# Kernel tuning notes

Measured on AMD Instinct MI355X. Metric: run time of the kernel, lower is better.

Reference implementation:

```python
import jax, jax.numpy as jnp
import numpy as np

E = 1024      # hidden_size
H = 16        # num_heads
D = E // H    # head_dim = 64
WIN = 256     # window_size
STRIDE = 128
G = 1         # global_tokens
B = 2
L = 4097      # seq_len; local_seq_len = 4096 tiles exactly into 31 windows


def setup_inputs() -> dict:
    key = jax.random.key(0)
    ks = jax.random.split(key, 9)
    s = 0.02
    return {
        "hidden_states": jax.random.normal(ks[0], (B, L, E), jnp.float32),
        "Wq": jax.random.normal(ks[1], (E, E), jnp.float32) * s,
        "bq": jnp.zeros((E,), jnp.float32),
        "Wk": jax.random.normal(ks[2], (E, E), jnp.float32) * s,
        "bk": jnp.zeros((E,), jnp.float32),
        "Wv": jax.random.normal(ks[3], (E, E), jnp.float32) * s,
        "bv": jnp.zeros((E,), jnp.float32),
        "Wo": jax.random.normal(ks[4], (E, E), jnp.float32) * s,
        "bo": jnp.zeros((E,), jnp.float32),
    }


def reference(hidden_states, Wq, bq, Wk, bk, Wv, bv, Wo, bo):
    b, seq_len, e = hidden_states.shape
    scale = 1.0 / jnp.sqrt(jnp.asarray(D, hidden_states.dtype))

    q = (hidden_states @ Wq + bq).reshape(b, seq_len, H, D)
    k = (hidden_states @ Wk + bk).reshape(b, seq_len, H, D)
    v = (hidden_states @ Wv + bv).reshape(b, seq_len, H, D)

    # ---- global tokens attend to the full sequence ----
    qg = q[:, :G]                                        # [b, G, H, D]
    gw = jnp.einsum('bghd,bshd->bhgs', qg, k) * scale    # [b, H, G, L]
    gp = jax.nn.softmax(gw, axis=-1)
    gctx = jnp.einsum('bhgs,bshd->bghd', gp, v).reshape(b, G, e)

    # ---- local windowed attention (overlapping strided windows) ----
    ql, kl, vl = q[:, G:], k[:, G:], v[:, G:]
    Lc = seq_len - G                                     # 4096
    num_windows = max(1, (Lc - WIN) // STRIDE + 1)       # 31
    starts = jnp.arange(num_windows) * STRIDE
    widx = starts[:, None] + jnp.arange(WIN)             # [W, w] window indices

    qw = ql[:, widx]                                     # [b, W, w, H, D]
    kw = kl[:, widx]
    vw = vl[:, widx]
    aw = jnp.einsum('bwqhd,bwkhd->bwhqk', qw, kw) * scale  # [b, W, H, w, w]
    ap = jax.nn.softmax(aw, axis=-1)
    ctx = jnp.einsum('bwhqk,bwkhd->bwqhd', ap, vw)       # [b, W, w, H, D]
    ctx = ctx.reshape(b, num_windows * WIN, e)

    flat = widx.reshape(-1)                              # [W*w]
    local = jnp.zeros((b, Lc, e), hidden_states.dtype).at[:, flat].add(ctx)
    counts = jnp.zeros((Lc,), hidden_states.dtype).at[flat].add(1.0)
    counts = jnp.maximum(counts, 1.0)
    local = local / counts[None, :, None]                # average over overlaps

    out = jnp.concatenate([gctx, local], axis=1)         # [b, L, E]
    return out @ Wo + bo
```

## Files before the change

kernel.cpp:

```cpp
#include <hip/hip_runtime.h>

typedef unsigned short u16;
typedef unsigned int u32;
typedef __bf16 bf16x8 __attribute__((ext_vector_type(8)));
typedef float f4_t __attribute__((ext_vector_type(4)));

#define E_DIM 1024
#define L_TOT 4097
#define B_SZ 2
#define M_ROWS 8194
#define NWIN 31
#define HHEADS 16
#define GCHUNKS 17

__device__ __forceinline__ float b2f(u16 v) {
  union { u32 u; float f; } x; x.u = ((u32)v) << 16; return x.f;
}
__device__ __forceinline__ u16 f2b(float f) {
  union { float f; u32 u; } x; x.f = f;
  u32 r = (x.u + 0x7FFFu + ((x.u >> 16) & 1u)) >> 16;
  return (u16)r;
}
__device__ __forceinline__ f4_t mfma16(bf16x8 a, bf16x8 b, f4_t c) {
  return __builtin_amdgcn_mfma_f32_16x16x32_bf16(a, b, c, 0, 0, 0);
}
__device__ __forceinline__ u32 cvtpk(float lo, float hi) {
  u32 r;
  asm volatile("v_cvt_pk_bf16_f32 %0, %1, %2" : "=v"(r) : "v"(lo), "v"(hi));
  return r;
}

#define GLOAD16(gp, lp)                                                              \
  __builtin_amdgcn_global_load_lds(                                                  \
      (const __attribute__((address_space(1))) u32*)(gp),                            \
      (__attribute__((address_space(3))) u32*)(lp), 16, 0, 0)

#define WAITVM(N) asm volatile("s_waitcnt vmcnt(" #N ")" ::: "memory")
#define WAITLGKM asm volatile("s_waitcnt lgkmcnt(0)" ::: "memory")
#define SCHEDB __builtin_amdgcn_sched_barrier(0)

__global__ __launch_bounds__(256) void prep_kernel(const float* __restrict__ hs,
                                                   u16* __restrict__ hsb,
                                                   const float* __restrict__ w0,
                                                   const float* __restrict__ w1,
                                                   const float* __restrict__ w2,
                                                   const float* __restrict__ w3,
                                                   u16* __restrict__ wtb) {
  int bid = blockIdx.x;
  if (bid < M_ROWS) {
    int i = bid * 256 + threadIdx.x;
    float4 v = ((const float4*)hs)[i];
    u16 o[4] = {f2b(v.x), f2b(v.y), f2b(v.z), f2b(v.w)};
    *(uint2*)(hsb + (size_t)i * 4) = *(uint2*)o;
  } else {
    int idx2 = bid - M_ROWS;
    int bz = idx2 >> 10;
    int rem = idx2 & 1023;
    int bx = rem & 31, by = rem >> 5;
    const float* src = bz == 0 ? w0 : bz == 1 ? w1 : bz == 2 ? w2 : w3;
    u16* dst = wtb + (size_t)bz * E_DIM * E_DIM;
    __shared__ float tile[32][33];
    int tx = threadIdx.x & 31, ty = threadIdx.x >> 5;
    int x = bx * 32 + tx;
    int y0 = by * 32;
    for (int j = ty; j < 32; j += 8) tile[j][tx] = src[(size_t)(y0 + j) * E_DIM + x];
    __syncthreads();
    for (int j = ty; j < 32; j += 8)
      dst[(size_t)(bx * 32 + j) * E_DIM + by * 32 + tx] = f2b(tile[tx][j]);
  }
}

template <int MODE>
__device__ __forceinline__ void gemmC_body(const u16* __restrict__ A,
                                           const u16* __restrict__ Wt,
                                           const float* __restrict__ b0,
                                           const float* __restrict__ b1,
                                           const float* __restrict__ b2,
                                           void* __restrict__ outBase,
                                           int M) {
  __shared__ __align__(16) char smraw[34816];
  u16* sA = (u16*)smraw;
  u16* sB = sA + 2 * 4096;
  u16* epi16 = (u16*)smraw;
  float* epi32 = (float*)smraw;

  int orig = blockIdx.x;
  int xcd = orig & 7, l = orig >> 3;
  int mt, nt;
  if (MODE == 0) {
    if (l < 192) { mt = (xcd << 3) + (l & 7); nt = l >> 3; }
    else         { mt = 64; nt = xcd * 3 + (l - 192); }
  } else {
    if (l < 64)  { mt = (xcd << 3) + (l & 7); nt = l >> 3; }
    else         { mt = 64; nt = xcd; }
  }
  int m0 = mt * 128, n0 = nt * 128;

  int t = threadIdx.x, lane = t & 63, w = t >> 6;
  int wr = w >> 1, wc = w & 1;
  int lr = lane & 15, g = lane >> 4;

  int ssrc = (((t & 3) ^ ((t >> 3) & 3)) << 3);
  const u16* pa[2];
  const u16* pb[2];
#pragma unroll
  for (int c = 0; c < 2; c++) {
    int ra = m0 + c * 64 + (t >> 2);
    if (ra >= M) ra = M - 1;
    pa[c] = A + (size_t)ra * 1024 + ssrc;
    pb[c] = Wt + (size_t)(n0 + c * 64 + (t >> 2)) * 1024 + ssrc;
  }
  int wb = w * 512;

#define STAGE(bf, ks)                                              \
  {                                                                \
    GLOAD16(pa[0] + (ks) * 32, sA + (bf) * 4096 + wb);             \
    GLOAD16(pa[1] + (ks) * 32, sA + (bf) * 4096 + 2048 + wb);      \
    GLOAD16(pb[0] + (ks) * 32, sB + (bf) * 4096 + wb);             \
    GLOAD16(pb[1] + (ks) * 32, sB + (bf) * 4096 + 2048 + wb);      \
  }

  int swz = ((g ^ ((lr >> 1) & 3)) << 3);
  int arow0 = wr * 64 + lr;
  int brow0 = wc * 64 + lr;

  f4_t acc[4][4] = {};

  STAGE(0, 0);
  STAGE(1, 1);
  WAITVM(4);
  __builtin_amdgcn_s_barrier();
  SCHEDB;

#pragma unroll 2
  for (int ks = 0; ks < 32; ++ks) {
    int bf = ks & 1;
    int base = bf * 4096;
    bf16x8 av[4], bv[4];
#pragma unroll
    for (int i = 0; i < 4; i++)
      av[i] = *(const bf16x8*)&sA[base + (arow0 + i * 16) * 32 + swz];
#pragma unroll
    for (int j = 0; j < 4; j++)
      bv[j] = *(const bf16x8*)&sB[base + (brow0 + j * 16) * 32 + swz];
    WAITLGKM;
    SCHEDB;
    __builtin_amdgcn_s_barrier();
    SCHEDB;
    if (ks < 30) STAGE(bf, ks + 2);
    SCHEDB;
    __builtin_amdgcn_s_setprio(1);
#pragma unroll
    for (int i = 0; i < 4; i++)
#pragma unroll
      for (int j = 0; j < 4; j++) acc[i][j] = mfma16(av[i], bv[j], acc[i][j]);
    __builtin_amdgcn_s_setprio(0);
    if (ks < 30) {
      WAITVM(4);
    } else if (ks == 30) {
      WAITVM(0);
    }
    if (ks < 31) {
      __builtin_amdgcn_s_barrier();
      SCHEDB;
    }
  }
  __syncthreads();

  if (MODE == 0) {
    int tsel = n0 >> 10, ncb = n0 & 1023;
    const float* bp = tsel == 0 ? b0 : (tsel == 1 ? b1 : b2);
#pragma unroll
    for (int j = 0; j < 4; j++) {
      int ncl = wc * 64 + j * 16 + lr;
      float bb = bp[ncb + ncl];
#pragma unroll
      for (int i = 0; i < 4; i++) {
        int mlb = wr * 64 + i * 16 + g * 4;
#pragma unroll
        for (int r = 0; r < 4; r++) epi16[(mlb + r) * 136 + ncl] = f2b(acc[i][j][r] + bb);
      }
    }
    __syncthreads();
    int row = t >> 1, half = t & 1;
    int m = m0 + row;
    if (m < M) {
      u16* op = (u16*)outBase + (size_t)tsel * ((size_t)M_ROWS * E_DIM) + (size_t)m * E_DIM + ncb + half * 64;
      const u16* lp = epi16 + row * 136 + half * 64;
#pragma unroll
      for (int qd = 0; qd < 8; qd++) ((uint4*)op)[qd] = ((const uint4*)lp)[qd];
    }
  } else {
#pragma unroll
    for (int p = 0; p < 2; p++) {
      if (p) __syncthreads();
      if (wc == p) {
#pragma unroll
        for (int j = 0; j < 4; j++) {
          int ncl = j * 16 + lr;
          float bb = b0[n0 + p * 64 + ncl];
#pragma unroll
          for (int i = 0; i < 4; i++) {
            int mlb = wr * 64 + i * 16 + g * 4;
#pragma unroll
            for (int r = 0; r < 4; r++) epi32[(mlb + r) * 68 + ncl] = acc[i][j][r] + bb;
          }
        }
      }
      __syncthreads();
      int row = t >> 1, qr = t & 1;
      int m = m0 + row;
      if (m < M) {
        float* op = (float*)outBase + (size_t)m * E_DIM + n0 + p * 64 + qr * 32;
        const float* lp = epi32 + row * 68 + qr * 32;
#pragma unroll
        for (int qd = 0; qd < 8; qd++) ((float4*)op)[qd] = ((const float4*)lp)[qd];
      }
    }
  }
#undef STAGE
}

__global__ __launch_bounds__(256, 4) void gemmC_qkv(const u16* __restrict__ A,
                                                    const u16* __restrict__ Wt,
                                                    const float* __restrict__ b0,
                                                    const float* __restrict__ b1,
                                                    const float* __restrict__ b2,
                                                    void* __restrict__ outBase,
                                                    int M) {
  gemmC_body<0>(A, Wt, b0, b1, b2, outBase, M);
}
__global__ __launch_bounds__(256, 4) void gemmC_out(const u16* __restrict__ A,
                                                    const u16* __restrict__ Wt,
                                                    const float* __restrict__ b0,
                                                    const float* __restrict__ b1,
                                                    const float* __restrict__ b2,
                                                    void* __restrict__ outBase,
                                                    int M) {
  gemmC_body<1>(A, Wt, b0, b1, b2, outBase, M);
}

#define VT_IDX(d, k) ((d) * 264 + ((k) ^ ((((d) >> 3) & 7) << 3)))
__global__ __launch_bounds__(256) void attn_fused(const u16* __restrict__ Qb,
                                                  const u16* __restrict__ Kb,
                                                  const u16* __restrict__ Vb,
                                                  float* __restrict__ part,
                                                  u16* __restrict__ winctx) {
  __shared__ __align__(16) char smem[66560];
  int bid = blockIdx.x;
  int t = threadIdx.x;

  if (bid < 544) {
    int c = bid % GCHUNKS;
    int rem = bid / GCHUNKS;
    int h = rem & 15, b = rem >> 4;
    float* qsh = (float*)smem;
    float* red = qsh + 64;
    float* psh = red + 4;
    float* cred = psh + 256;

    size_t base = (size_t)b * L_TOT * E_DIM + h * 64;
    if (t < 64) qsh[t] = b2f(Qb[base + t]);
    __syncthreads();

    int row = c * 256 + t;
    bool valid = row < L_TOT;
    float dot = -1e30f;
    if (valid) {
      const u16* kp = Kb + base + (size_t)row * E_DIM;
      float acc = 0.f;
#pragma unroll
      for (int j = 0; j < 64; j += 8) {
        uint4 kv = *(const uint4*)(kp + j);
        const u16* kk = (const u16*)&kv;
#pragma unroll
        for (int q = 0; q < 8; q++) acc += qsh[j + q] * b2f(kk[q]);
      }
      dot = acc * 0.125f;
    }
    float m = dot;
    for (int mask = 1; mask < 64; mask <<= 1) m = fmaxf(m, __shfl_xor(m, mask));
    if ((t & 63) == 0) red[t >> 6] = m;
    __syncthreads();
    m = fmaxf(fmaxf(red[0], red[1]), fmaxf(red[2], red[3]));
    float p = valid ? __expf(dot - m) : 0.f;
    psh[t] = p;
    float s = p;
    for (int mask = 1; mask < 64; mask <<= 1) s += __shfl_xor(s, mask);
    __syncthreads();
    if ((t & 63) == 0) red[t >> 6] = s;
    __syncthreads();
    s = red[0] + red[1] + red[2] + red[3];

    int d = t & 63, gq = t >> 6;
    float acc = 0.f;
#pragma unroll 4
    for (int i = 0; i < 64; i++) {
      int sl = gq * 64 + i;
      int r2 = c * 256 + sl;
      if (r2 < L_TOT) acc += psh[sl] * b2f(Vb[base + (size_t)r2 * E_DIM + d]);
    }
    cred[gq * 64 + d] = acc;
    __syncthreads();
    if (t < 64) {
      float v = cred[t] + cred[64 + t] + cred[128 + t] + cred[192 + t];
      float* pp = part + (((size_t)(b * HHEADS + h) * GCHUNKS + c) * 66);
      pp[t] = v;
      if (t == 0) { pp[64] = m; pp[65] = s; }
    }
    return;
  }

  int id = bid - 544;
  int wdw = id % NWIN;
  int rem = id / NWIN;
  int h = rem & 15, b = rem >> 4;

  u16* Ks = (u16*)smem;
  u16* Vt = Ks + 256 * 64;

  int lane = t & 63, wv = t >> 6;
  int g = lane >> 4, lr = lane & 15;
  size_t rowbase = (size_t)b * L_TOT + 1 + (size_t)wdw * 128;
  int hoff = h * 64;

  {
    int rsub = t >> 3;
    int ssrc = ((t & 7) ^ (rsub & 7)) * 8;
    const u16* kp = Kb + (rowbase + rsub) * E_DIM + hoff + ssrc;
#pragma unroll
    for (int c = 0; c < 8; c++)
      GLOAD16(kp + (size_t)c * 32 * E_DIM, Ks + c * 2048 + wv * 512);
  }
#pragma unroll
  for (int rep = 0; rep < 8; rep++) {
    int u = rep * 256 + t;
    int i = u >> 3;
    int d0 = (u & 7) * 8;
    uint4 v = *(const uint4*)(Vb + (rowbase + i) * E_DIM + hoff + d0);
    const u16* pv = (const u16*)&v;
#pragma unroll
    for (int j = 0; j < 8; j++) Vt[VT_IDX(d0 + j, i)] = pv[j];
  }
  __syncthreads();

  int slo = (2 * (g & 1)) * 16 + lr;
  int shi = slo + 16;

  for (int grp = 0; grp < 4; grp++) {
    int q0 = grp * 64 + wv * 16;
    const u16* qp = Qb + (rowbase + q0 + lr) * E_DIM + hoff;
    bf16x8 qa0 = *(const bf16x8*)(qp + g * 8);
    bf16x8 qa1 = *(const bf16x8*)(qp + 32 + g * 8);

    f4_t s[16];
    __builtin_amdgcn_s_setprio(1);
#pragma unroll
    for (int ki = 0; ki < 16; ki++) {
      int row = ki * 16 + lr;
      bf16x8 ka0 = *(const bf16x8*)&Ks[row * 64 + ((g ^ (lr & 7)) << 3)];
      bf16x8 ka1 = *(const bf16x8*)&Ks[row * 64 + (((4 + g) ^ (lr & 7)) << 3)];
      f4_t z = {};
      z = mfma16(ka0, qa0, z);
      z = mfma16(ka1, qa1, z);
      s[ki] = z;
    }
    __builtin_amdgcn_s_setprio(0);

    float mx = -1e30f;
#pragma unroll
    for (int ki = 0; ki < 16; ki++) {
      mx = fmaxf(mx, fmaxf(fmaxf(s[ki][0], s[ki][1]), fmaxf(s[ki][2], s[ki][3])));
    }
    mx = fmaxf(mx, __shfl_xor(mx, 16));
    mx = fmaxf(mx, __shfl_xor(mx, 32));
    float mx8 = mx * 0.125f;
    float sum = 0.f;
    u32 pk[16][2];
#pragma unroll
    for (int ki = 0; ki < 16; ki++) {
      float p0 = __expf(fmaf(s[ki][0], 0.125f, -mx8));
      float p1 = __expf(fmaf(s[ki][1], 0.125f, -mx8));
      float p2 = __expf(fmaf(s[ki][2], 0.125f, -mx8));
      float p3 = __expf(fmaf(s[ki][3], 0.125f, -mx8));
      sum += (p0 + p1) + (p2 + p3);
      pk[ki][0] = cvtpk(p0, p1);
      pk[ki][1] = cvtpk(p2, p3);
    }
    sum += __shfl_xor(sum, 16);
    sum += __shfl_xor(sum, 32);
    float inv = 1.0f / sum;

    u32 paw[8][4];
    bool hi = g >= 2;
#pragma unroll
    for (int kt = 0; kt < 8; kt++) {
      u32 v00 = __shfl((int)pk[kt * 2][0], slo);
      u32 v01 = __shfl((int)pk[kt * 2][1], slo);
      u32 v10 = __shfl((int)pk[kt * 2 + 1][0], slo);
      u32 v11 = __shfl((int)pk[kt * 2 + 1][1], slo);
      u32 w00 = __shfl((int)pk[kt * 2][0], shi);
      u32 w01 = __shfl((int)pk[kt * 2][1], shi);
      u32 w10 = __shfl((int)pk[kt * 2 + 1][0], shi);
      u32 w11 = __shfl((int)pk[kt * 2 + 1][1], shi);
      paw[kt][0] = hi ? v10 : v00;
      paw[kt][1] = hi ? v11 : v01;
      paw[kt][2] = hi ? w10 : w00;
      paw[kt][3] = hi ? w11 : w01;
    }

    f4_t o[4] = {};
    __builtin_amdgcn_s_setprio(1);
#pragma unroll
    for (int dtile = 0; dtile < 4; dtile++) {
      int d = dtile * 16 + lr;
      int dswz = (((d >> 3) & 7) << 3);
#pragma unroll
      for (int kt = 0; kt < 8; kt++) {
        int kphys = (kt * 32 + g * 8) ^ dswz;
        bf16x8 vb = *(const bf16x8*)&Vt[d * 264 + kphys];
        o[dtile] = mfma16(*(const bf16x8*)&paw[kt][0], vb, o[dtile]);
      }
    }
    __builtin_amdgcn_s_setprio(0);

    float invr[4];
#pragma unroll
    for (int r = 0; r < 4; r++) invr[r] = __shfl(inv, g * 4 + r);
    size_t orow = (size_t)(b * NWIN + wdw) * 256 + q0;
#pragma unroll
    for (int dtile = 0; dtile < 4; dtile++) {
#pragma unroll
      for (int r = 0; r < 4; r++) {
        winctx[(orow + g * 4 + r) * E_DIM + hoff + dtile * 16 + lr] =
            f2b(o[dtile][r] * invr[r]);
      }
    }
  }
}

__global__ __launch_bounds__(256) void combine2_kernel(const u16* __restrict__ winctx,
                                                       const float* __restrict__ part,
                                                       u16* __restrict__ ctxb) {
  if (blockIdx.x == 4096) {
    for (int i = threadIdx.x; i < 2048; i += 256) {
      int bh = i >> 6, d = i & 63;
      int b = bh >> 4, h = bh & 15;
      const float* pp = part + ((size_t)(b * HHEADS + h) * GCHUNKS) * 66;
      float m = -1e30f;
#pragma unroll
      for (int c = 0; c < GCHUNKS; c++) m = fmaxf(m, pp[c * 66 + 64]);
      float stot = 0.f, acc = 0.f;
#pragma unroll
      for (int c = 0; c < GCHUNKS; c++) {
        float w = __expf(pp[c * 66 + 64] - m);
        stot += pp[c * 66 + 65] * w;
        acc += pp[c * 66 + d] * w;
      }
      ctxb[(size_t)b * L_TOT * E_DIM + h * 64 + d] = f2b(acc / stot);
    }
    return;
  }
  int idx = blockIdx.x * 256 + threadIdx.x;
  int e0 = (idx & 127) * 8;
  int p = (idx >> 7) & 4095;
  int b = idx >> 19;
  int whi = p >> 7;
  if (whi > 30) whi = 30;
  int off_hi = p - whi * 128;
  int wlo = whi - 1;
  bool has_lo = (wlo >= 0) && (off_hi < 128);

  uint4 vhi = *(const uint4*)(winctx + (((size_t)(b * NWIN + whi) * 256 + off_hi) * E_DIM) + e0);
  const u16* ph = (const u16*)&vhi;
  float vals[8];
#pragma unroll
  for (int j = 0; j < 8; j++) vals[j] = b2f(ph[j]);
  if (has_lo) {
    uint4 vlo = *(const uint4*)(winctx + (((size_t)(b * NWIN + wlo) * 256 + off_hi + 128) * E_DIM) + e0);
    const u16* pl = (const u16*)&vlo;
#pragma unroll
    for (int j = 0; j < 8; j++) vals[j] = (vals[j] + b2f(pl[j])) * 0.5f;
  }
  u16 out[8];
#pragma unroll
  for (int j = 0; j < 8; j++) out[j] = f2b(vals[j]);
  *(uint4*)(ctxb + ((size_t)b * L_TOT + 1 + p) * E_DIM + e0) = *(uint4*)out;
}

extern "C" void kernel_launch(void* const* d_in, const int* in_sizes, int n_in,
                              void* d_out, int out_size, void* d_ws, size_t ws_size,
                              hipStream_t stream) {
  const float* hs = (const float*)d_in[0];
  const float* Wq = (const float*)d_in[1];
  const float* bq = (const float*)d_in[2];
  const float* Wk = (const float*)d_in[3];
  const float* bk = (const float*)d_in[4];
  const float* Wv = (const float*)d_in[5];
  const float* bv = (const float*)d_in[6];
  const float* Wo = (const float*)d_in[7];
  const float* bo = (const float*)d_in[8];

  const size_t BLE = (size_t)M_ROWS * E_DIM;
  const size_t BLE_B = BLE * 2;
  const size_t EE = (size_t)E_DIM * E_DIM;

  char* ws = (char*)d_ws;
  u16* hsb = (u16*)(ws);
  u16* wtb = (u16*)(ws + BLE_B);
  u16* qkv = (u16*)(ws + BLE_B + 4 * EE * 2);
  u16* Qb = qkv;
  u16* Kb = qkv + BLE;
  u16* Vb = qkv + 2 * BLE;
  u16* ctxb = (u16*)(ws + BLE_B + 4 * EE * 2 + 3 * BLE_B);
  u16* winctx = (u16*)(ws + BLE_B + 4 * EE * 2 + 4 * BLE_B);
  float* gpart = (float*)(ws + BLE_B + 4 * EE * 2 + 4 * BLE_B +
                          (size_t)B_SZ * NWIN * 256 * E_DIM * 2);

  prep_kernel<<<M_ROWS + 4096, 256, 0, stream>>>(hs, hsb, Wq, Wk, Wv, Wo, wtb);
  gemmC_qkv<<<1560, 256, 0, stream>>>(hsb, wtb, bq, bk, bv, qkv, M_ROWS);
  attn_fused<<<1536, 256, 0, stream>>>(Qb, Kb, Vb, gpart, winctx);
  combine2_kernel<<<4097, 256, 0, stream>>>(winctx, gpart, ctxb);
  gemmC_out<<<520, 256, 0, stream>>>(ctxb, wtb + 3 * EE, bo, bo, bo, d_out, M_ROWS);
}
```

Baseline: 206.6 us.

## Widen QKV GEMM tile to 128x256 with dedicated kernel

Replaces the templated 128x128 QKV projection GEMM with a dedicated kernel using 128x256 output tiles. Each wave computes 4x8 MFMA blocks, and shared memory grows to 48KB with launch bounds of 2 blocks per CU. The grid drops from 1560 to 784 blocks, and the epilogue writes its bf16 output in two halves. The aim is more reuse of each loaded A tile per MFMA and less global/LDS traffic, at the cost of higher register pressure, lower occupancy and a possibly worse wave tail.

```diff
diff --git a/kernel.cpp b/kernel.cpp
--- a/kernel.cpp
+++ b/kernel.cpp
@@ -70,30 +70,148 @@
   }
 }
 
-template <int MODE>
-__device__ __forceinline__ void gemmC_body(const u16* __restrict__ A,
-                                           const u16* __restrict__ Wt,
-                                           const float* __restrict__ b0,
-                                           const float* __restrict__ b1,
-                                           const float* __restrict__ b2,
-                                           void* __restrict__ outBase,
-                                           int M) {
+__global__ __launch_bounds__(256, 2) void gemmF_qkv(const u16* __restrict__ A,
+                                                    const u16* __restrict__ Wt,
+                                                    const float* __restrict__ b0,
+                                                    const float* __restrict__ b1,
+                                                    const float* __restrict__ b2,
+                                                    void* __restrict__ outBase,
+                                                    int M) {
+  __shared__ __align__(16) char smraw[49152];
+  u16* sA = (u16*)smraw;
+  u16* sB = sA + 2 * 4096;
+  u16* epi16 = (u16*)smraw;
+
+  int orig = blockIdx.x;
+  int xcd = orig & 7, l = orig >> 3;
+  int mt, nt;
+  if (l < 96)      { mt = (xcd << 3) + (l & 7); nt = l >> 3; }
+  else if (l == 96){ mt = 64; nt = xcd; }
+  else             { if (xcd >= 4) return; mt = 64; nt = 8 + xcd; }
+  int m0 = mt * 128, n0 = nt * 256;
+
+  int t = threadIdx.x, lane = t & 63, w = t >> 6;
+  int wr = w >> 1, wc = w & 1;
+  int lr = lane & 15, g = lane >> 4;
+
+  int ssrc = (((t & 3) ^ ((t >> 3) & 3)) << 3);
+  const u16* pa[2];
+  const u16* pb[4];
+#pragma unroll
+  for (int c = 0; c < 2; c++) {
+    int ra = m0 + c * 64 + (t >> 2);
+    if (ra >= M) ra = M - 1;
+    pa[c] = A + (size_t)ra * 1024 + ssrc;
+  }
+#pragma unroll
+  for (int c = 0; c < 4; c++)
+    pb[c] = Wt + (size_t)(n0 + c * 64 + (t >> 2)) * 1024 + ssrc;
+  int wb = w * 512;
+
+#define STAGE(bf, ks)                                              \
+  {                                                                \
+    GLOAD16(pa[0] + (ks) * 32, sA + (bf) * 4096 + wb);             \
+    GLOAD16(pa[1] + (ks) * 32, sA + (bf) * 4096 + 2048 + wb);      \
+    GLOAD16(pb[0] + (ks) * 32, sB + (bf) * 8192 + wb);             \
+    GLOAD16(pb[1] + (ks) * 32, sB + (bf) * 8192 + 2048 + wb);      \
+    GLOAD16(pb[2] + (ks) * 32, sB + (bf) * 8192 + 4096 + wb);      \
+    GLOAD16(pb[3] + (ks) * 32, sB + (bf) * 8192 + 6144 + wb);      \
+  }
+
+  int swz = ((g ^ ((lr >> 1) & 3)) << 3);
+  int arow0 = wr * 64 + lr;
+  int brow0 = wc * 128 + lr;
+
+  f4_t acc[4][8] = {};
+
+  STAGE(0, 0);
+  STAGE(1, 1);
+  WAITVM(6);
+  __builtin_amdgcn_s_barrier();
+  SCHEDB;
+
+#pragma unroll 2
+  for (int ks = 0; ks < 32; ++ks) {
+    int bf = ks & 1;
+    int baseA = bf * 4096, baseB = bf * 8192;
+    bf16x8 av[4], bv[8];
+#pragma unroll
+    for (int i = 0; i < 4; i++)
+      av[i] = *(const bf16x8*)&sA[baseA + (arow0 + i * 16) * 32 + swz];
+#pragma unroll
+    for (int j = 0; j < 8; j++)
+      bv[j] = *(const bf16x8*)&sB[baseB + (brow0 + j * 16) * 32 + swz];
+    WAITLGKM;
+    SCHEDB;
+    __builtin_amdgcn_s_barrier();
+    SCHEDB;
+    if (ks < 30) STAGE(bf, ks + 2);
+    SCHEDB;
+    __builtin_amdgcn_s_setprio(1);
+#pragma unroll
+    for (int i = 0; i < 4; i++)
+#pragma unroll
+      for (int j = 0; j < 8; j++) acc[i][j] = mfma16(av[i], bv[j], acc[i][j]);
+    __builtin_amdgcn_s_setprio(0);
+    if (ks < 30) {
+      WAITVM(6);
+    } else if (ks == 30) {
+      WAITVM(0);
+    }
+    if (ks < 31) {
+      __builtin_amdgcn_s_barrier();
+      SCHEDB;
+    }
+  }
+  __syncthreads();
+
+  int tsel = n0 >> 10, ncb = n0 & 1023;
+  const float* bp = tsel == 0 ? b0 : (tsel == 1 ? b1 : b2);
+  u16* outp = (u16*)outBase + (size_t)tsel * ((size_t)M_ROWS * E_DIM);
+#pragma unroll
+  for (int p = 0; p < 2; p++) {
+    if (p) __syncthreads();
+    if (wc == p) {
+#pragma unroll
+      for (int j = 0; j < 8; j++) {
+        int ncl = j * 16 + lr;
+        float bb = bp[ncb + p * 128 + ncl];
+#pragma unroll
+        for (int i = 0; i < 4; i++) {
+          int mlb = wr * 64 + i * 16 + g * 4;
+#pragma unroll
+          for (int r = 0; r < 4; r++) epi16[(mlb + r) * 136 + ncl] = f2b(acc[i][j][r] + bb);
+        }
+      }
+    }
+    __syncthreads();
+    int row = t >> 1, half = t & 1;
+    int m = m0 + row;
+    if (m < M) {
+      u16* op = outp + (size_t)m * E_DIM + ncb + p * 128 + half * 64;
+      const u16* lp = epi16 + row * 136 + half * 64;
+#pragma unroll
+      for (int qd = 0; qd < 8; qd++) ((uint4*)op)[qd] = ((const uint4*)lp)[qd];
+    }
+  }
+#undef STAGE
+}
+
+__global__ __launch_bounds__(256, 4) void gemmC_out(const u16* __restrict__ A,
+                                                    const u16* __restrict__ Wt,
+                                                    const float* __restrict__ b0,
+                                                    void* __restrict__ outBase,
+                                                    int M) {
   __shared__ __align__(16) char smraw[34816];
   u16* sA = (u16*)smraw;
   u16* sB = sA + 2 * 4096;
-  u16* epi16 = (u16*)smraw;
   float* epi32 = (float*)smraw;
 
   int orig = blockIdx.x;
   int xcd = orig & 7, l = orig >> 3;
   int mt, nt;
-  if (MODE == 0) {
-    if (l < 192) { mt = (xcd << 3) + (l & 7); nt = l >> 3; }
-    else         { mt = 64; nt = xcd * 3 + (l - 192); }
-  } else {
-    if (l < 64)  { mt = (xcd << 3) + (l & 7); nt = l >> 3; }
-    else         { mt = 64; nt = xcd; }
-  }
+  if (l < 64)  { mt = (xcd << 3) + (l & 7); nt = l >> 3; }
+  else         { mt = 64; nt = xcd; }
   int m0 = mt * 128, n0 = nt * 128;
 
   int t = threadIdx.x, lane = t & 63, w = t >> 6;
@@ -167,77 +285,33 @@
   }
   __syncthreads();
 
-  if (MODE == 0) {
-    int tsel = n0 >> 10, ncb = n0 & 1023;
-    const float* bp = tsel == 0 ? b0 : (tsel == 1 ? b1 : b2);
-#pragma unroll
-    for (int j = 0; j < 4; j++) {
-      int ncl = wc * 64 + j * 16 + lr;
-      float bb = bp[ncb + ncl];
-#pragma unroll
-      for (int i = 0; i < 4; i++) {
-        int mlb = wr * 64 + i * 16 + g * 4;
-#pragma unroll
-        for (int r = 0; r < 4; r++) epi16[(mlb + r) * 136 + ncl] = f2b(acc[i][j][r] + bb);
+#pragma unroll
+  for (int p = 0; p < 2; p++) {
+    if (p) __syncthreads();
+    if (wc == p) {
+#pragma unroll
+      for (int j = 0; j < 4; j++) {
+        int ncl = j * 16 + lr;
+        float bb = b0[n0 + p * 64 + ncl];
+#pragma unroll
+        for (int i = 0; i < 4; i++) {
+          int mlb = wr * 64 + i * 16 + g * 4;
+#pragma unroll
+          for (int r = 0; r < 4; r++) epi32[(mlb + r) * 68 + ncl] = acc[i][j][r] + bb;
+        }
       }
     }
     __syncthreads();
-    int row = t >> 1, half = t & 1;
+    int row = t >> 1, qr = t & 1;
     int m = m0 + row;
     if (m < M) {
-      u16* op = (u16*)outBase + (size_t)tsel * ((size_t)M_ROWS * E_DIM) + (size_t)m * E_DIM + ncb + half * 64;
-      const u16* lp = epi16 + row * 136 + half * 64;
-#pragma unroll
-      for (int qd = 0; qd < 8; qd++) ((uint4*)op)[qd] = ((const uint4*)lp)[qd];
-    }
-  } else {
-#pragma unroll
-    for (int p = 0; p < 2; p++) {
-      if (p) __syncthreads();
-      if (wc == p) {
-#pragma unroll
-        for (int j = 0; j < 4; j++) {
-          int ncl = j * 16 + lr;
-          float bb = b0[n0 + p * 64 + ncl];
-#pragma unroll
-          for (int i = 0; i < 4; i++) {
-            int mlb = wr * 64 + i * 16 + g * 4;
-#pragma unroll
-            for (int r = 0; r < 4; r++) epi32[(mlb + r) * 68 + ncl] = acc[i][j][r] + bb;
-          }
-        }
-      }
-      __syncthreads();
-      int row = t >> 1, qr = t & 1;
-      int m = m0 + row;
-      if (m < M) {
-        float* op = (float*)outBase + (size_t)m * E_DIM + n0 + p * 64 + qr * 32;
-        const float* lp = epi32 + row * 68 + qr * 32;
-#pragma unroll
-        for (int qd = 0; qd < 8; qd++) ((float4*)op)[qd] = ((const float4*)lp)[qd];
-      }
+      float* op = (float*)outBase + (size_t)m * E_DIM + n0 + p * 64 + qr * 32;
+      const float* lp = epi32 + row * 68 + qr * 32;
+#pragma unroll
+      for (int qd = 0; qd < 8; qd++) ((float4*)op)[qd] = ((const float4*)lp)[qd];
     }
   }
 #undef STAGE
-}
-
-__global__ __launch_bounds__(256, 4) void gemmC_qkv(const u16* __restrict__ A,
-                                                    const u16* __restrict__ Wt,
-                                                    const float* __restrict__ b0,
-                                                    const float* __restrict__ b1,
-                                                    const float* __restrict__ b2,
-                                                    void* __restrict__ outBase,
-                                                    int M) {
-  gemmC_body<0>(A, Wt, b0, b1, b2, outBase, M);
-}
-__global__ __launch_bounds__(256, 4) void gemmC_out(const u16* __restrict__ A,
-                                                    const u16* __restrict__ Wt,
-                                                    const float* __restrict__ b0,
-                                                    const float* __restrict__ b1,
-                                                    const float* __restrict__ b2,
-                                                    void* __restrict__ outBase,
-                                                    int M) {
-  gemmC_body<1>(A, Wt, b0, b1, b2, outBase, M);
 }
 
 #define VT_IDX(d, k) ((d) * 264 + ((k) ^ ((((d) >> 3) & 7) << 3)))
@@ -518,8 +592,8 @@
                           (size_t)B_SZ * NWIN * 256 * E_DIM * 2);
 
   prep_kernel<<<M_ROWS + 4096, 256, 0, stream>>>(hs, hsb, Wq, Wk, Wv, Wo, wtb);
-  gemmC_qkv<<<1560, 256, 0, stream>>>(hsb, wtb, bq, bk, bv, qkv, M_ROWS);
+  gemmF_qkv<<<784, 256, 0, stream>>>(hsb, wtb, bq, bk, bv, qkv, M_ROWS);
   attn_fused<<<1536, 256, 0, stream>>>(Qb, Kb, Vb, gpart, winctx);
   combine2_kernel<<<4097, 256, 0, stream>>>(winctx, gpart, ctxb);
-  gemmC_out<<<520, 256, 0, stream>>>(ctxb, wtb + 3 * EE, bo, bo, bo, d_out, M_ROWS);
-}
+  gemmC_out<<<520, 256, 0, stream>>>(ctxb, wtb + 3 * EE, bo, d_out, M_ROWS);
+}
```

New measurement: 203.7 us (median of 2 runs). No clear change (-1.4%).

## Replace LDS-staged QKV GEMM with single-wave register-direct GEMM

Applied to the files above, without the earlier changes.

The QKV projection GEMM is replaced with a one-wavefront-per-block kernel computing a 64x128 tile. Operands are loaded directly from global memory into registers for MFMA, with no LDS staging, barriers or software pipelining. This aims to remove shared-memory and synchronization overhead and raise block count. In exchange it loses LDS data reuse, relies on cache bandwidth, and uses a larger per-wave accumulator footprint.

```diff
diff --git a/kernel.cpp b/kernel.cpp
--- a/kernel.cpp
+++ b/kernel.cpp
@@ -70,30 +70,95 @@
   }
 }
 
-template <int MODE>
-__device__ __forceinline__ void gemmC_body(const u16* __restrict__ A,
-                                           const u16* __restrict__ Wt,
-                                           const float* __restrict__ b0,
-                                           const float* __restrict__ b1,
-                                           const float* __restrict__ b2,
-                                           void* __restrict__ outBase,
-                                           int M) {
+__global__ __launch_bounds__(64, 4) void gemmR_qkv(const u16* __restrict__ A,
+                                                   const u16* __restrict__ Wt,
+                                                   const float* __restrict__ b0,
+                                                   const float* __restrict__ b1,
+                                                   const float* __restrict__ b2,
+                                                   void* __restrict__ outBase,
+                                                   int M) {
+  __shared__ __align__(16) u16 epi[64 * 136];
+
+  int orig = blockIdx.x;
+  int xcd = orig & 7, l = orig >> 3;
+  int mt, nt;
+  if (l < 384) { mt = (xcd << 4) + (l & 15); nt = l >> 4; }
+  else         { mt = 128; nt = xcd * 3 + (l - 384); }
+  int m0 = mt * 64, n0 = nt * 128;
+
+  int lane = threadIdx.x;
+  int g = lane >> 4, lr = lane & 15;
+
+  const u16* pa[4];
+  const u16* pb[8];
+#pragma unroll
+  for (int i = 0; i < 4; i++) {
+    int r = m0 + i * 16 + lr;
+    if (r >= M) r = M - 1;
+    pa[i] = A + (size_t)r * 1024 + g * 8;
+  }
+#pragma unroll
+  for (int j = 0; j < 8; j++)
+    pb[j] = Wt + (size_t)(n0 + j * 16 + lr) * 1024 + g * 8;
+
+  f4_t acc[4][8] = {};
+
+#pragma unroll 4
+  for (int ks = 0; ks < 32; ++ks) {
+    bf16x8 av[4], bv[8];
+#pragma unroll
+    for (int i = 0; i < 4; i++) av[i] = *(const bf16x8*)(pa[i] + ks * 32);
+#pragma unroll
+    for (int j = 0; j < 8; j++) bv[j] = *(const bf16x8*)(pb[j] + ks * 32);
+#pragma unroll
+    for (int i = 0; i < 4; i++)
+#pragma unroll
+      for (int j = 0; j < 8; j++) acc[i][j] = mfma16(av[i], bv[j], acc[i][j]);
+  }
+
+  int tsel = n0 >> 10, ncb = n0 & 1023;
+  const float* bp = tsel == 0 ? b0 : (tsel == 1 ? b1 : b2);
+  u16* outp = (u16*)outBase + (size_t)tsel * ((size_t)M_ROWS * E_DIM);
+#pragma unroll
+  for (int j = 0; j < 8; j++) {
+    int ncl = j * 16 + lr;
+    float bb = bp[ncb + ncl];
+#pragma unroll
+    for (int i = 0; i < 4; i++) {
+#pragma unroll
+      for (int r = 0; r < 4; r++)
+        epi[(i * 16 + g * 4 + r) * 136 + ncl] = f2b(acc[i][j][r] + bb);
+    }
+  }
+  WAITLGKM;
+  SCHEDB;
+#pragma unroll
+  for (int p = 0; p < 16; p++) {
+    int row = p * 4 + (lane >> 4);
+    int chunk = lane & 15;
+    int m = m0 + row;
+    if (m < M) {
+      *(uint4*)(outp + (size_t)m * E_DIM + ncb + chunk * 8) =
+          *(const uint4*)(epi + row * 136 + chunk * 8);
+    }
+  }
+}
+
+__global__ __launch_bounds__(256, 4) void gemmC_out(const u16* __restrict__ A,
+                                                    const u16* __restrict__ Wt,
+                                                    const float* __restrict__ b0,
+                                                    void* __restrict__ outBase,
+                                                    int M) {
   __shared__ __align__(16) char smraw[34816];
   u16* sA = (u16*)smraw;
   u16* sB = sA + 2 * 4096;
-  u16* epi16 = (u16*)smraw;
   float* epi32 = (float*)smraw;
 
   int orig = blockIdx.x;
   int xcd = orig & 7, l = orig >> 3;
   int mt, nt;
-  if (MODE == 0) {
-    if (l < 192) { mt = (xcd << 3) + (l & 7); nt = l >> 3; }
-    else         { mt = 64; nt = xcd * 3 + (l - 192); }
-  } else {
-    if (l < 64)  { mt = (xcd << 3) + (l & 7); nt = l >> 3; }
-    else         { mt = 64; nt = xcd; }
-  }
+  if (l < 64)  { mt = (xcd << 3) + (l & 7); nt = l >> 3; }
+  else         { mt = 64; nt = xcd; }
   int m0 = mt * 128, n0 = nt * 128;
 
   int t = threadIdx.x, lane = t & 63, w = t >> 6;
@@ -167,77 +232,33 @@
   }
   __syncthreads();
 
-  if (MODE == 0) {
-    int tsel = n0 >> 10, ncb = n0 & 1023;
-    const float* bp = tsel == 0 ? b0 : (tsel == 1 ? b1 : b2);
-#pragma unroll
-    for (int j = 0; j < 4; j++) {
-      int ncl = wc * 64 + j * 16 + lr;
-      float bb = bp[ncb + ncl];
-#pragma unroll
-      for (int i = 0; i < 4; i++) {
-        int mlb = wr * 64 + i * 16 + g * 4;
-#pragma unroll
-        for (int r = 0; r < 4; r++) epi16[(mlb + r) * 136 + ncl] = f2b(acc[i][j][r] + bb);
+#pragma unroll
+  for (int p = 0; p < 2; p++) {
+    if (p) __syncthreads();
+    if (wc == p) {
+#pragma unroll
+      for (int j = 0; j < 4; j++) {
+        int ncl = j * 16 + lr;
+        float bb = b0[n0 + p * 64 + ncl];
+#pragma unroll
+        for (int i = 0; i < 4; i++) {
+          int mlb = wr * 64 + i * 16 + g * 4;
+#pragma unroll
+          for (int r = 0; r < 4; r++) epi32[(mlb + r) * 68 + ncl] = acc[i][j][r] + bb;
+        }
       }
     }
     __syncthreads();
-    int row = t >> 1, half = t & 1;
+    int row = t >> 1, qr = t & 1;
     int m = m0 + row;
     if (m < M) {
-      u16* op = (u16*)outBase + (size_t)tsel * ((size_t)M_ROWS * E_DIM) + (size_t)m * E_DIM + ncb + half * 64;
-      const u16* lp = epi16 + row * 136 + half * 64;
-#pragma unroll
-      for (int qd = 0; qd < 8; qd++) ((uint4*)op)[qd] = ((const uint4*)lp)[qd];
-    }
-  } else {
-#pragma unroll
-    for (int p = 0; p < 2; p++) {
-      if (p) __syncthreads();
-      if (wc == p) {
-#pragma unroll
-        for (int j = 0; j < 4; j++) {
-          int ncl = j * 16 + lr;
-          float bb = b0[n0 + p * 64 + ncl];
-#pragma unroll
-          for (int i = 0; i < 4; i++) {
-            int mlb = wr * 64 + i * 16 + g * 4;
-#pragma unroll
-            for (int r = 0; r < 4; r++) epi32[(mlb + r) * 68 + ncl] = acc[i][j][r] + bb;
-          }
-        }
-      }
-      __syncthreads();
-      int row = t >> 1, qr = t & 1;
-      int m = m0 + row;
-      if (m < M) {
-        float* op = (float*)outBase + (size_t)m * E_DIM + n0 + p * 64 + qr * 32;
-        const float* lp = epi32 + row * 68 + qr * 32;
-#pragma unroll
-        for (int qd = 0; qd < 8; qd++) ((float4*)op)[qd] = ((const float4*)lp)[qd];
-      }
+      float* op = (float*)outBase + (size_t)m * E_DIM + n0 + p * 64 + qr * 32;
+      const float* lp = epi32 + row * 68 + qr * 32;
+#pragma unroll
+      for (int qd = 0; qd < 8; qd++) ((float4*)op)[qd] = ((const float4*)lp)[qd];
     }
   }
 #undef STAGE
-}
-
-__global__ __launch_bounds__(256, 4) void gemmC_qkv(const u16* __restrict__ A,
-                                                    const u16* __restrict__ Wt,
-                                                    const float* __restrict__ b0,
-                                                    const float* __restrict__ b1,
-                                                    const float* __restrict__ b2,
-                                                    void* __restrict__ outBase,
-                                                    int M) {
-  gemmC_body<0>(A, Wt, b0, b1, b2, outBase, M);
-}
-__global__ __launch_bounds__(256, 4) void gemmC_out(const u16* __restrict__ A,
-                                                    const u16* __restrict__ Wt,
-                                                    const float* __restrict__ b0,
-                                                    const float* __restrict__ b1,
-                                                    const float* __restrict__ b2,
-                                                    void* __restrict__ outBase,
-                                                    int M) {
-  gemmC_body<1>(A, Wt, b0, b1, b2, outBase, M);
 }
 
 #define VT_IDX(d, k) ((d) * 264 + ((k) ^ ((((d) >> 3) & 7) << 3)))
@@ -518,8 +539,8 @@
                           (size_t)B_SZ * NWIN * 256 * E_DIM * 2);
 
   prep_kernel<<<M_ROWS + 4096, 256, 0, stream>>>(hs, hsb, Wq, Wk, Wv, Wo, wtb);
-  gemmC_qkv<<<1560, 256, 0, stream>>>(hsb, wtb, bq, bk, bv, qkv, M_ROWS);
+  gemmR_qkv<<<3096, 64, 0, stream>>>(hsb, wtb, bq, bk, bv, qkv, M_ROWS);
   attn_fused<<<1536, 256, 0, stream>>>(Qb, Kb, Vb, gpart, winctx);
   combine2_kernel<<<4097, 256, 0, stream>>>(winctx, gpart, ctxb);
-  gemmC_out<<<520, 256, 0, stream>>>(ctxb, wtb + 3 * EE, bo, bo, bo, d_out, M_ROWS);
-}
+  gemmC_out<<<520, 256, 0, stream>>>(ctxb, wtb + 3 * EE, bo, d_out, M_ROWS);
+}
```

After: 314.3 us. +52.1%, slower.
